# Kernel optimization log

Measured on AMD Instinct MI355X. Metric: run time of the kernel, lower is better.

## Reference

```python
import jax, jax.numpy as jnp
import numpy as np

N_NODES = 50000
N_EDGES = 800000
IN_CH = 128
HID = 256


def gcn_layer(x, src, dst, W, b, n_nodes):
    # x: [N, F_in] -> h: [N, F_out]
    h = x @ W
    # add self loops (PyG GCNConv default)
    loop = jnp.arange(n_nodes, dtype=src.dtype)
    src_f = jnp.concatenate([src, loop])
    dst_f = jnp.concatenate([dst, loop])
    # symmetric normalization: deg^{-1/2}[src] * deg^{-1/2}[dst]
    deg = jax.ops.segment_sum(jnp.ones_like(dst_f, dtype=h.dtype), dst_f, num_segments=n_nodes)
    dinv = jnp.where(deg > 0, jax.lax.rsqrt(deg), 0.0)
    norm = dinv[src_f] * dinv[dst_f]  # [E+N]
    msg = h[src_f] * norm[:, None]    # [E+N, F_out] gather
    out = jax.ops.segment_sum(msg, dst_f, num_segments=n_nodes)  # scatter-add
    return out + b


def setup_inputs() -> dict:
    key = jax.random.key(0)
    k1, k2, k3, k4 = jax.random.split(key, 4)
    x = jax.random.normal(k1, (N_NODES, IN_CH), dtype=jnp.float32)
    edge_index = jax.random.randint(k2, (2, N_EDGES), 0, N_NODES, dtype=jnp.int64)
    W1 = jax.random.normal(k3, (IN_CH, HID), dtype=jnp.float32) * (1.0 / np.sqrt(IN_CH))
    b1 = jnp.zeros((HID,), dtype=jnp.float32)
    W2 = jax.random.normal(k4, (HID, HID), dtype=jnp.float32) * (1.0 / np.sqrt(HID))
    b2 = jnp.zeros((HID,), dtype=jnp.float32)
    return {"x": x, "edge_index": edge_index, "W1": W1, "b1": b1, "W2": W2, "b2": b2}


def reference(x, edge_index, W1, b1, W2, b2):
    src, dst = edge_index[0], edge_index[1]
    h = gcn_layer(x, src, dst, W1, b1, N_NODES)
    h = jax.nn.relu(h)
    # dropout in eval mode (training=False) is identity
    out = gcn_layer(h, src, dst, W2, b2, N_NODES)
    return out
```

## Files before the change

kernel.cpp:

```cpp
#include <hip/hip_runtime.h>

constexpr int N = 50000;
constexpr int E = 800000;
constexpr int NPAD = 50048;
constexpr int NB = (N + 255) / 256;

typedef _Float16 half8 __attribute__((ext_vector_type(8)));
typedef _Float16 half4v __attribute__((ext_vector_type(4)));
typedef float float4v __attribute__((ext_vector_type(4)));

__global__ __launch_bounds__(256) void deg_kernel(const int* __restrict__ dst,
                                                  int* __restrict__ degI) {
    int e = blockIdx.x * 256 + threadIdx.x;
    if (e < E) atomicAdd(&degI[dst[e]], 1);
}

__global__ __launch_bounds__(256) void dinv_kernel(const int* __restrict__ degI,
                                                   float* __restrict__ dinv) {
    int v = blockIdx.x * 256 + threadIdx.x;
    if (v < N) dinv[v] = rsqrtf((float)degI[v] + 1.0f);
}

__global__ __launch_bounds__(256) void scan1_kernel(const int* __restrict__ degI,
                                                    int* __restrict__ incl,
                                                    int* __restrict__ blockSums) {
    __shared__ int s[256];
    int t = threadIdx.x;
    int i = blockIdx.x * 256 + t;
    int d = (i < N) ? degI[i] : 0;
    s[t] = d;
    __syncthreads();
    for (int off = 1; off < 256; off <<= 1) {
        int v = s[t];
        int u = (t >= off) ? s[t - off] : 0;
        __syncthreads();
        s[t] = v + u;
        __syncthreads();
    }
    if (i < N) incl[i] = s[t];
    if (t == 255) blockSums[blockIdx.x] = s[255];
}

__global__ __launch_bounds__(256) void scan2_kernel(int* __restrict__ blockSums) {
    __shared__ int s[256];
    int t = threadIdx.x;
    int v = (t < NB) ? blockSums[t] : 0;
    s[t] = v;
    __syncthreads();
    for (int off = 1; off < 256; off <<= 1) {
        int a = s[t];
        int u = (t >= off) ? s[t - off] : 0;
        __syncthreads();
        s[t] = a + u;
        __syncthreads();
    }
    if (t < NB) blockSums[t] = s[t] - v;
}

__global__ __launch_bounds__(256) void scan3_kernel(const int* __restrict__ degI,
                                                    const int* __restrict__ incl,
                                                    const int* __restrict__ blockSums,
                                                    int* __restrict__ rowptr,
                                                    int* __restrict__ cursor) {
    int i = blockIdx.x * 256 + threadIdx.x;
    if (i < N) {
        int e = blockSums[blockIdx.x] + incl[i] - degI[i];
        rowptr[i] = e;
        cursor[i] = e;
    }
    if (i == 0) rowptr[N] = E;
}

__global__ __launch_bounds__(256) void fill_kernel(const int* __restrict__ src,
                                                   const int* __restrict__ dst,
                                                   int* __restrict__ cursor,
                                                   int* __restrict__ eidx) {
    int e = blockIdx.x * 256 + threadIdx.x;
    if (e >= E) return;
    int d = dst[e];
    int pos = atomicAdd(&cursor[d], 1);
    eidx[pos] = src[e];
}

template <int K>
__global__ __launch_bounds__(256) void wt_kernel(const float* __restrict__ W,
                                                 _Float16* __restrict__ Wt) {
    int idx = blockIdx.x * 256 + threadIdx.x;
    int k = idx & (K - 1);
    int n = idx >> (K == 128 ? 7 : 8);
    Wt[idx] = (_Float16)W[(size_t)k * 256 + n];
}

__global__ __launch_bounds__(256) void prescale_kernel(const float4* __restrict__ x,
                                                       const float* __restrict__ dinv,
                                                       half4v* __restrict__ px) {
    int idx = blockIdx.x * 256 + threadIdx.x;
    if (idx >= N * 32) return;
    float dv = dinv[idx >> 5];
    float4 t = x[idx];
    half4v o;
    o[0] = (_Float16)(t.x * dv);
    o[1] = (_Float16)(t.y * dv);
    o[2] = (_Float16)(t.z * dv);
    o[3] = (_Float16)(t.w * dv);
    px[idx] = o;
}

template <int T>
__global__ __launch_bounds__(256) void aggregate_chunked(
    const int* __restrict__ rowptr, const int* __restrict__ eidx,
    const half4v* __restrict__ f, const float* __restrict__ dinv,
    half4v* __restrict__ q) {
    constexpr int NCHUNK = T / 32;
    constexpr int NSEG = 8 / NCHUNK;
    constexpr int SEGN = N / NSEG;
    constexpr int RS = T / 4;

    const int slot = blockIdx.x & 7;
    const int chunk = slot & (NCHUNK - 1);
    const int seg = slot / NCHUNK;
    const int sub = threadIdx.x >> 3;
    const int cl = threadIdx.x & 7;
    const int v = seg * SEGN + (blockIdx.x >> 3) * 32 + sub;
    if (v >= seg * SEGN + SEGN) return;

    const int coff = chunk * 8 + cl;

    half4v s = f[(size_t)v * RS + coff];
    float a0 = (float)s[0], a1 = (float)s[1], a2 = (float)s[2], a3 = (float)s[3];

    int i = rowptr[v];
    const int end = rowptr[v + 1];
    for (; i + 4 <= end; i += 4) {
        int e0 = eidx[i + 0], e1 = eidx[i + 1], e2 = eidx[i + 2], e3 = eidx[i + 3];
        half4v t0 = f[(size_t)e0 * RS + coff];
        half4v t1 = f[(size_t)e1 * RS + coff];
        half4v t2 = f[(size_t)e2 * RS + coff];
        half4v t3 = f[(size_t)e3 * RS + coff];
        a0 += ((float)t0[0] + (float)t1[0]) + ((float)t2[0] + (float)t3[0]);
        a1 += ((float)t0[1] + (float)t1[1]) + ((float)t2[1] + (float)t3[1]);
        a2 += ((float)t0[2] + (float)t1[2]) + ((float)t2[2] + (float)t3[2]);
        a3 += ((float)t0[3] + (float)t1[3]) + ((float)t2[3] + (float)t3[3]);
    }
    for (; i < end; ++i) {
        half4v t = f[(size_t)eidx[i] * RS + coff];
        a0 += (float)t[0];
        a1 += (float)t[1];
        a2 += (float)t[2];
        a3 += (float)t[3];
    }

    float dv = dinv[v];
    half4v o;
    o[0] = (_Float16)(a0 * dv);
    o[1] = (_Float16)(a1 * dv);
    o[2] = (_Float16)(a2 * dv);
    o[3] = (_Float16)(a3 * dv);
    q[(size_t)v * RS + coff] = o;
}

template <int K, bool FUSE1>
__global__ __launch_bounds__(256) void gemm_mfma(
    const _Float16* __restrict__ A, const _Float16* __restrict__ Wt,
    const float* __restrict__ bias, const float* __restrict__ dinv,
    void* __restrict__ outp) {
    constexpr int LSTR = K + 8;
    __shared__ _Float16 Bs[64 * LSTR];

    const int tid = threadIdx.x;
    const int wave = tid >> 6;
    const int lane = tid & 63;
    const int m = lane & 15;
    const int quad = lane >> 4;
    const int rbase = blockIdx.x * 64 + wave * 16;
    const int row = rbase + m;

    half8 af[K / 32];
    {
        const half8* Arow = (const half8*)(A + (size_t)row * K);
#pragma unroll
        for (int i = 0; i < K / 32; ++i) af[i] = Arow[i * 4 + quad];
    }

    for (int cc = 0; cc < 4; ++cc) {
        const int colbase = cc * 64;
        if (cc) __syncthreads();
        {
            int col = tid >> 2;
            int sub = tid & 3;
            const half8* srcb = (const half8*)(Wt + (size_t)(colbase + col) * K);
            half8* dstb = (half8*)&Bs[col * LSTR];
#pragma unroll
            for (int u = 0; u < K / 32; ++u) dstb[sub + u * 4] = srcb[sub + u * 4];
        }
        __syncthreads();

        float4v acc[4] = {};
#pragma unroll
        for (int k0 = 0; k0 < K; k0 += 32) {
            half8 a = af[k0 >> 5];
#pragma unroll
            for (int c = 0; c < 4; ++c) {
                half8 b = *(const half8*)&Bs[(c * 16 + m) * LSTR + k0 + quad * 8];
                acc[c] = __builtin_amdgcn_mfma_f32_16x16x32_f16(a, b, acc[c], 0, 0, 0);
            }
        }

#pragma unroll
        for (int c = 0; c < 4; ++c) {
            int col = colbase + c * 16 + m;
            float bcol = bias[col];
#pragma unroll
            for (int r = 0; r < 4; ++r) {
                int orow = rbase + quad * 4 + r;
                if (orow < N) {
                    float val = acc[c][r] + bcol;
                    if (FUSE1) {
                        val = fmaxf(val, 0.f) * dinv[orow];
                        ((_Float16*)outp)[(size_t)orow * 256 + col] = (_Float16)val;
                    } else {
                        ((float*)outp)[(size_t)orow * 256 + col] = val;
                    }
                }
            }
        }
    }
}

extern "C" void kernel_launch(void* const* d_in, const int* in_sizes, int n_in,
                              void* d_out, int out_size, void* d_ws, size_t ws_size,
                              hipStream_t stream) {
    const float* x  = (const float*)d_in[0];
    const int* edge = (const int*)d_in[1];
    const int* src  = edge;
    const int* dst  = edge + E;
    const float* W1 = (const float*)d_in[2];
    const float* b1 = (const float*)d_in[3];
    const float* W2 = (const float*)d_in[4];
    const float* b2 = (const float*)d_in[5];
    float* out = (float*)d_out;

    _Float16* bufA = (_Float16*)d_ws;
    _Float16* bufB = bufA + (size_t)NPAD * 256;
    float* dinv    = (float*)(bufB + (size_t)NPAD * 256);
    int* degI      = (int*)(dinv + N);
    int* rowptr    = degI + N;
    int* cursor    = rowptr + (N + 1);
    int* eidx      = cursor + N;
    _Float16* W1t  = (_Float16*)(eidx + E);
    _Float16* W2t  = W1t + 256 * 128;
    int* blockSums = (int*)(W2t + 256 * 256);

    hipMemsetAsync(degI, 0, N * sizeof(int), stream);
    deg_kernel<<<(E + 255) / 256, 256, 0, stream>>>(dst, degI);
    dinv_kernel<<<(N + 255) / 256, 256, 0, stream>>>(degI, dinv);
    scan1_kernel<<<NB, 256, 0, stream>>>(degI, cursor, blockSums);
    scan2_kernel<<<1, 256, 0, stream>>>(blockSums);
    scan3_kernel<<<NB, 256, 0, stream>>>(degI, cursor, blockSums, rowptr, cursor);
    fill_kernel<<<(E + 255) / 256, 256, 0, stream>>>(src, dst, cursor, eidx);

    wt_kernel<128><<<(256 * 128) / 256, 256, 0, stream>>>(W1, W1t);
    wt_kernel<256><<<(256 * 256) / 256, 256, 0, stream>>>(W2, W2t);

    prescale_kernel<<<(N * 32 + 255) / 256, 256, 0, stream>>>(
        (const float4*)x, dinv, (half4v*)bufA);
    aggregate_chunked<128><<<8 * ((N / 2 + 31) / 32), 256, 0, stream>>>(
        rowptr, eidx, (const half4v*)bufA, dinv, (half4v*)bufB);
    gemm_mfma<128, true><<<NPAD / 64, 256, 0, stream>>>(
        bufB, W1t, b1, dinv, bufA);

    aggregate_chunked<256><<<8 * ((N + 31) / 32), 256, 0, stream>>>(
        rowptr, eidx, (const half4v*)bufA, dinv, (half4v*)bufB);
    gemm_mfma<256, false><<<NPAD / 64, 256, 0, stream>>>(
        bufB, W2t, b2, dinv, out);
}
```

Baseline: 353.4 us.

## Replace chunked half4 aggregation with wide half8 per-node gather

```diff
diff --git a/kernel.cpp b/kernel.cpp
--- a/kernel.cpp
+++ b/kernel.cpp
@@ -107,56 +107,60 @@
 }
 
 template <int T>
-__global__ __launch_bounds__(256) void aggregate_chunked(
+__global__ __launch_bounds__(256) void aggregate_wide(
     const int* __restrict__ rowptr, const int* __restrict__ eidx,
-    const half4v* __restrict__ f, const float* __restrict__ dinv,
-    half4v* __restrict__ q) {
-    constexpr int NCHUNK = T / 32;
-    constexpr int NSEG = 8 / NCHUNK;
-    constexpr int SEGN = N / NSEG;
-    constexpr int RS = T / 4;
-
-    const int slot = blockIdx.x & 7;
-    const int chunk = slot & (NCHUNK - 1);
-    const int seg = slot / NCHUNK;
-    const int sub = threadIdx.x >> 3;
-    const int cl = threadIdx.x & 7;
-    const int v = seg * SEGN + (blockIdx.x >> 3) * 32 + sub;
-    if (v >= seg * SEGN + SEGN) return;
-
-    const int coff = chunk * 8 + cl;
-
-    half4v s = f[(size_t)v * RS + coff];
-    float a0 = (float)s[0], a1 = (float)s[1], a2 = (float)s[2], a3 = (float)s[3];
+    const half8* __restrict__ f, const float* __restrict__ dinv,
+    half8* __restrict__ q) {
+    constexpr int LPN = T / 8;
+    constexpr int NPB = 256 / LPN;
+
+    const int v = blockIdx.x * NPB + threadIdx.x / LPN;
+    if (v >= N) return;
+    const int lane = threadIdx.x % LPN;
+    const size_t base = (size_t)v * LPN + lane;
+
+    half8 s = f[base];
+    float a[8];
+#pragma unroll
+    for (int j = 0; j < 8; ++j) a[j] = (float)s[j];
 
     int i = rowptr[v];
     const int end = rowptr[v + 1];
-    for (; i + 4 <= end; i += 4) {
+    for (; i + 8 <= end; i += 8) {
         int e0 = eidx[i + 0], e1 = eidx[i + 1], e2 = eidx[i + 2], e3 = eidx[i + 3];
-        half4v t0 = f[(size_t)e0 * RS + coff];
-        half4v t1 = f[(size_t)e1 * RS + coff];
-        half4v t2 = f[(size_t)e2 * RS + coff];
-        half4v t3 = f[(size_t)e3 * RS + coff];
-        a0 += ((float)t0[0] + (float)t1[0]) + ((float)t2[0] + (float)t3[0]);
-        a1 += ((float)t0[1] + (float)t1[1]) + ((float)t2[1] + (float)t3[1]);
-        a2 += ((float)t0[2] + (float)t1[2]) + ((float)t2[2] + (float)t3[2]);
-        a3 += ((float)t0[3] + (float)t1[3]) + ((float)t2[3] + (float)t3[3]);
-    }
-    for (; i < end; ++i) {
-        half4v t = f[(size_t)eidx[i] * RS + coff];
-        a0 += (float)t[0];
-        a1 += (float)t[1];
-        a2 += (float)t[2];
-        a3 += (float)t[3];
+        int e4 = eidx[i + 4], e5 = eidx[i + 5], e6 = eidx[i + 6], e7 = eidx[i + 7];
+        half8 t0 = f[(size_t)e0 * LPN + lane];
+        half8 t1 = f[(size_t)e1 * LPN + lane];
+        half8 t2 = f[(size_t)e2 * LPN + lane];
+        half8 t3 = f[(size_t)e3 * LPN + lane];
+        half8 t4 = f[(size_t)e4 * LPN + lane];
+        half8 t5 = f[(size_t)e5 * LPN + lane];
+        half8 t6 = f[(size_t)e6 * LPN + lane];
+        half8 t7 = f[(size_t)e7 * LPN + lane];
+#pragma unroll
+        for (int j = 0; j < 8; ++j) {
+            a[j] += (((float)t0[j] + (float)t1[j]) + ((float)t2[j] + (float)t3[j])) +
+                    (((float)t4[j] + (float)t5[j]) + ((float)t6[j] + (float)t7[j]));
+        }
+    }
+    for (; i + 2 <= end; i += 2) {
+        int e0 = eidx[i], e1 = eidx[i + 1];
+        half8 t0 = f[(size_t)e0 * LPN + lane];
+        half8 t1 = f[(size_t)e1 * LPN + lane];
+#pragma unroll
+        for (int j = 0; j < 8; ++j) a[j] += (float)t0[j] + (float)t1[j];
+    }
+    if (i < end) {
+        half8 t0 = f[(size_t)eidx[i] * LPN + lane];
+#pragma unroll
+        for (int j = 0; j < 8; ++j) a[j] += (float)t0[j];
     }
 
     float dv = dinv[v];
-    half4v o;
-    o[0] = (_Float16)(a0 * dv);
-    o[1] = (_Float16)(a1 * dv);
-    o[2] = (_Float16)(a2 * dv);
-    o[3] = (_Float16)(a3 * dv);
-    q[(size_t)v * RS + coff] = o;
+    half8 o;
+#pragma unroll
+    for (int j = 0; j < 8; ++j) o[j] = (_Float16)(a[j] * dv);
+    q[base] = o;
 }
 
 template <int K, bool FUSE1>
@@ -264,13 +268,13 @@
 
     prescale_kernel<<<(N * 32 + 255) / 256, 256, 0, stream>>>(
         (const float4*)x, dinv, (half4v*)bufA);
-    aggregate_chunked<128><<<8 * ((N / 2 + 31) / 32), 256, 0, stream>>>(
-        rowptr, eidx, (const half4v*)bufA, dinv, (half4v*)bufB);
+    aggregate_wide<128><<<(N + 15) / 16, 256, 0, stream>>>(
+        rowptr, eidx, (const half8*)bufA, dinv, (half8*)bufB);
     gemm_mfma<128, true><<<NPAD / 64, 256, 0, stream>>>(
         bufB, W1t, b1, dinv, bufA);
 
-    aggregate_chunked<256><<<8 * ((N + 31) / 32), 256, 0, stream>>>(
-        rowptr, eidx, (const half4v*)bufA, dinv, (half4v*)bufB);
+    aggregate_wide<256><<<(N + 7) / 8, 256, 0, stream>>>(
+        rowptr, eidx, (const half8*)bufA, dinv, (half8*)bufB);
     gemm_mfma<256, false><<<NPAD / 64, 256, 0, stream>>>(
         bufB, W2t, b2, dinv, out);
 }
```

After: 323.5 us. 1.09x faster.
